# Kernel optimization log

Measured on AMD Instinct MI355X. Metric: run time of the kernel, lower is better.

The kernel has to match this reference:

```python
import jax, jax.numpy as jnp
import numpy as np

NUM_SAMPLE = 10


def setup_inputs() -> dict:
    key = jax.random.key(0)
    k1, k2, k3, k4, k5 = jax.random.split(key, 5)
    N, F, B, S = 100000, 256, 20000, NUM_SAMPLE
    features_ue = jax.random.normal(k1, (N, F), dtype=jnp.float32)
    features_ap = jax.random.normal(k2, (N, F), dtype=jnp.float32)
    neigh_idx = jax.random.randint(k3, (B, S), 0, N, dtype=jnp.int32)
    nodes = jax.random.randint(k4, (B,), 0, N, dtype=jnp.int32)
    # xavier-uniform weight [embed_dim, feature_dim] = [256, 2*F]
    embed_dim, feature_dim = 256, 2 * F
    limit = float(np.sqrt(6.0 / (embed_dim + feature_dim)))
    weight = jax.random.uniform(k5, (embed_dim, feature_dim), dtype=jnp.float32,
                                minval=-limit, maxval=limit)
    return {"features_ue": features_ue, "features_ap": features_ap,
            "neigh_idx": neigh_idx, "nodes": nodes, "weight": weight}


def reference(features_ue, features_ap, neigh_idx, nodes, weight):
    # sample_model='ue2ue': other_feature = self_feature = features_ue
    S = neigh_idx.shape[1]
    # gather sampled neighbor features: [B, S, F] -> sum over S
    gathered = jnp.take(features_ue, neigh_idx, axis=0)
    # original: mask.div(num_neigh + 1), i.e. divide by count PLUS one
    neigh_feats = gathered.sum(axis=1) / jnp.float32(S + 1)  # [B, F]
    self_feats = jnp.take(features_ue, nodes, axis=0)        # [B, F]
    combined = jnp.concatenate([self_feats, neigh_feats], axis=1)  # [B, 2F]
    # weight.mm(combined.t()) then relu -> [embed_dim, B]
    out = jax.nn.relu(jnp.einsum('ef,bf->eb', weight, combined))
    return out
```

## Files before the change

kernel.cpp:

```cpp
#include <hip/hip_runtime.h>

typedef __attribute__((ext_vector_type(8))) short short8;
typedef __attribute__((ext_vector_type(4))) float f32x4;

#define B_TOTAL 20000
#define B_PAD   20096
#define NF      256
#define K2      512
#define NS      10

__device__ __forceinline__ unsigned short f2bf(float x) {
    unsigned u = __builtin_bit_cast(unsigned, x);
    u += 0x7FFFu + ((u >> 16) & 1u);
    return (unsigned short)(u >> 16);
}

__global__ __launch_bounds__(256) void gather_combine(
    const float* __restrict__ ue, const int* __restrict__ nidx,
    const int* __restrict__ nodes, const float* __restrict__ w,
    unsigned short* __restrict__ comb, unsigned short* __restrict__ wbf)
{
    const int t = threadIdx.x, blk = blockIdx.x;
    if (blk < 128) {
        const int base = blk * 1024 + t * 4;
        const float4 v = *(const float4*)(w + base);
        ushort4 o;
        o.x = f2bf(v.x); o.y = f2bf(v.y); o.z = f2bf(v.z); o.w = f2bf(v.w);
        *(ushort4*)(wbf + base) = o;
    }
    const int lane = t & 63;
    const int b = blk * 4 + (t >> 6);
    if (b >= B_PAD) return;
    unsigned short* crow = comb + (size_t)b * K2;
    if (b < B_TOTAL) {
        const int node = nodes[b];
        const float4 sf = ((const float4*)(ue + (size_t)node * NF))[lane];
        int myidx = 0;
        if (lane < NS) myidx = nidx[b * NS + lane];
        float ax = 0.f, ay = 0.f, az = 0.f, aw = 0.f;
        #pragma unroll
        for (int s = 0; s < NS; ++s) {
            const int is = __shfl(myidx, s);
            const float4 v = ((const float4*)(ue + (size_t)is * NF))[lane];
            ax += v.x; ay += v.y; az += v.z; aw += v.w;
        }
        const float inv = 1.0f / 11.0f;
        ushort4 s4, n4;
        s4.x = f2bf(sf.x); s4.y = f2bf(sf.y); s4.z = f2bf(sf.z); s4.w = f2bf(sf.w);
        n4.x = f2bf(ax * inv); n4.y = f2bf(ay * inv); n4.z = f2bf(az * inv); n4.w = f2bf(aw * inv);
        *(ushort4*)(crow + lane * 4) = s4;
        *(ushort4*)(crow + NF + lane * 4) = n4;
    } else {
        ushort4 z; z.x = z.y = z.z = z.w = 0;
        *(ushort4*)(crow + lane * 4) = z;
        *(ushort4*)(crow + NF + lane * 4) = z;
    }
}

__global__ __launch_bounds__(256) void gemm_relu(
    const unsigned short* __restrict__ wbf,
    const unsigned short* __restrict__ comb,
    float* __restrict__ out)
{
    __shared__ unsigned short Alds[4096];
    __shared__ unsigned short Blds[4096];
    const int t    = threadIdx.x;
    const int lane = t & 63;
    const int wv   = t >> 6;
    const int wm   = wv >> 1, wn = wv & 1;
    const int n0   = blockIdx.x * 128;
    const int m0   = blockIdx.y * 128;
    const int srow = t & 127;
    const int skg  = t >> 7;
    const int fr   = lane & 15;
    const int kq   = lane >> 4;

    f32x4 acc[4][4] = {};

    const short8* A8 = (const short8*)Alds;
    const short8* B8 = (const short8*)Blds;

    for (int ks = 0; ks < 16; ++ks) {
        const unsigned short* ga = wbf  + (size_t)(m0 + srow) * K2 + ks * 32 + skg * 8;
        const unsigned short* gb = comb + (size_t)(n0 + srow) * K2 + ks * 32 + skg * 8;
        unsigned short* la = Alds + t * 8;
        unsigned short* lb = Blds + t * 8;
        __builtin_amdgcn_global_load_lds((const __attribute__((address_space(1))) void*)ga,
            (__attribute__((address_space(3))) void*)la, 16, 0, 0);
        __builtin_amdgcn_global_load_lds((const __attribute__((address_space(1))) void*)(ga + 16),
            (__attribute__((address_space(3))) void*)(la + 2048), 16, 0, 0);
        __builtin_amdgcn_global_load_lds((const __attribute__((address_space(1))) void*)gb,
            (__attribute__((address_space(3))) void*)lb, 16, 0, 0);
        __builtin_amdgcn_global_load_lds((const __attribute__((address_space(1))) void*)(gb + 16),
            (__attribute__((address_space(3))) void*)(lb + 2048), 16, 0, 0);
        asm volatile("s_waitcnt vmcnt(0)" ::: "memory");
        __syncthreads();

        short8 af[4], bg[4];
        #pragma unroll
        for (int i = 0; i < 4; ++i)
            af[i] = A8[kq * 128 + wm * 64 + i * 16 + fr];
        #pragma unroll
        for (int j = 0; j < 4; ++j)
            bg[j] = B8[kq * 128 + wn * 64 + j * 16 + fr];
        #pragma unroll
        for (int i = 0; i < 4; ++i)
            #pragma unroll
            for (int j = 0; j < 4; ++j)
                acc[i][j] = __builtin_amdgcn_mfma_f32_16x16x32_bf16(af[i], bg[j], acc[i][j], 0, 0, 0);
        __syncthreads();
    }

    #pragma unroll
    for (int i = 0; i < 4; ++i) {
        const int e = m0 + wm * 64 + i * 16 + kq * 4;
        #pragma unroll
        for (int j = 0; j < 4; ++j) {
            const int b = n0 + wn * 64 + j * 16 + fr;
            if (b < B_TOTAL) {
                #pragma unroll
                for (int r = 0; r < 4; ++r)
                    out[(size_t)(e + r) * B_TOTAL + b] = fmaxf(acc[i][j][r], 0.0f);
            }
        }
    }
}

extern "C" void kernel_launch(void* const* d_in, const int* in_sizes, int n_in,
                              void* d_out, int out_size, void* d_ws, size_t ws_size,
                              hipStream_t stream) {
    const float* ue    = (const float*)d_in[0];
    const int*   nidx  = (const int*)d_in[2];
    const int*   nodes = (const int*)d_in[3];
    const float* w     = (const float*)d_in[4];
    float*       out   = (float*)d_out;

    unsigned short* comb = (unsigned short*)d_ws;
    unsigned short* wbf  = comb + (size_t)B_PAD * K2;

    hipLaunchKernelGGL(gather_combine, dim3(B_PAD / 4), dim3(256), 0, stream,
                       ue, nidx, nodes, w, comb, wbf);
    hipLaunchKernelGGL(gemm_relu, dim3(B_PAD / 128, 2), dim3(256), 0, stream,
                       wbf, comb, out);
}
```

Measured before the change: 60.64 us.

## Restructure GEMM to stage full-K comb tile in LDS and read weights from global

Each block now covers a 64-column slice of comb and computes all 256 output rows. The block loads its full K=512 comb tile into LDS once, in two halves, and starts MFMAs on the first half while the second half is still arriving. Weight fragments are read directly from global memory (L2-resident) instead of being staged in LDS. This removes the per-K-step sync and LDS staging loop and means comb is read once rather than twice. In exchange it uses 64KB of LDS per block, which limits occupancy, and relies on global-memory latency for the weight loads.

```diff
diff --git a/kernel.cpp b/kernel.cpp
--- a/kernel.cpp
+++ b/kernel.cpp
@@ -47,7 +47,8 @@
         const float inv = 1.0f / 11.0f;
         ushort4 s4, n4;
         s4.x = f2bf(sf.x); s4.y = f2bf(sf.y); s4.z = f2bf(sf.z); s4.w = f2bf(sf.w);
-        n4.x = f2bf(ax * inv); n4.y = f2bf(ay * inv); n4.z = f2bf(az * inv); n4.w = f2bf(aw * inv);
+        n4.x = f2bf(ax * inv); n4.y = f2bf(ay * inv);
+        n4.z = f2bf(az * inv); n4.w = f2bf(aw * inv);
         *(ushort4*)(crow + lane * 4) = s4;
         *(ushort4*)(crow + NF + lane * 4) = n4;
     } else {
@@ -62,61 +63,74 @@
     const unsigned short* __restrict__ comb,
     float* __restrict__ out)
 {
-    __shared__ unsigned short Alds[4096];
-    __shared__ unsigned short Blds[4096];
+    __shared__ unsigned short Blds[64 * K2];
     const int t    = threadIdx.x;
     const int lane = t & 63;
     const int wv   = t >> 6;
-    const int wm   = wv >> 1, wn = wv & 1;
-    const int n0   = blockIdx.x * 128;
-    const int m0   = blockIdx.y * 128;
-    const int srow = t & 127;
-    const int skg  = t >> 7;
+    const int n0   = blockIdx.x * 64;
     const int fr   = lane & 15;
     const int kq   = lane >> 4;
 
+    #pragma unroll
+    for (int L = 0; L < 16; ++L) {
+        const int kg = L * 4 + wv;
+        const unsigned short* src = comb + (size_t)(n0 + lane) * K2 + kg * 8;
+        __builtin_amdgcn_global_load_lds(
+            (const __attribute__((address_space(1))) void*)src,
+            (__attribute__((address_space(3))) void*)(Blds + ((size_t)kg * 64 + lane) * 8),
+            16, 0, 0);
+    }
+
+    asm volatile("s_waitcnt vmcnt(8)" ::: "memory");
+    __builtin_amdgcn_s_barrier();
+    __builtin_amdgcn_sched_barrier(0);
+
+    const unsigned short* wp = wbf + (size_t)(wv * 64 + fr) * K2 + kq * 8;
+    const short8* B8 = (const short8*)Blds;
     f32x4 acc[4][4] = {};
 
-    const short8* A8 = (const short8*)Alds;
-    const short8* B8 = (const short8*)Blds;
-
-    for (int ks = 0; ks < 16; ++ks) {
-        const unsigned short* ga = wbf  + (size_t)(m0 + srow) * K2 + ks * 32 + skg * 8;
-        const unsigned short* gb = comb + (size_t)(n0 + srow) * K2 + ks * 32 + skg * 8;
-        unsigned short* la = Alds + t * 8;
-        unsigned short* lb = Blds + t * 8;
-        __builtin_amdgcn_global_load_lds((const __attribute__((address_space(1))) void*)ga,
-            (__attribute__((address_space(3))) void*)la, 16, 0, 0);
-        __builtin_amdgcn_global_load_lds((const __attribute__((address_space(1))) void*)(ga + 16),
-            (__attribute__((address_space(3))) void*)(la + 2048), 16, 0, 0);
-        __builtin_amdgcn_global_load_lds((const __attribute__((address_space(1))) void*)gb,
-            (__attribute__((address_space(3))) void*)lb, 16, 0, 0);
-        __builtin_amdgcn_global_load_lds((const __attribute__((address_space(1))) void*)(gb + 16),
-            (__attribute__((address_space(3))) void*)(lb + 2048), 16, 0, 0);
-        asm volatile("s_waitcnt vmcnt(0)" ::: "memory");
-        __syncthreads();
-
+    #pragma unroll 4
+    for (int ks = 0; ks < 8; ++ks) {
         short8 af[4], bg[4];
         #pragma unroll
         for (int i = 0; i < 4; ++i)
-            af[i] = A8[kq * 128 + wm * 64 + i * 16 + fr];
+            af[i] = *(const short8*)(wp + (size_t)i * 16 * K2 + ks * 32);
         #pragma unroll
         for (int j = 0; j < 4; ++j)
-            bg[j] = B8[kq * 128 + wn * 64 + j * 16 + fr];
+            bg[j] = B8[(ks * 4 + kq) * 64 + j * 16 + fr];
         #pragma unroll
         for (int i = 0; i < 4; ++i)
             #pragma unroll
             for (int j = 0; j < 4; ++j)
                 acc[i][j] = __builtin_amdgcn_mfma_f32_16x16x32_bf16(af[i], bg[j], acc[i][j], 0, 0, 0);
-        __syncthreads();
+    }
+
+    asm volatile("s_waitcnt vmcnt(0)" ::: "memory");
+    __builtin_amdgcn_s_barrier();
+    __builtin_amdgcn_sched_barrier(0);
+
+    #pragma unroll 4
+    for (int ks = 8; ks < 16; ++ks) {
+        short8 af[4], bg[4];
+        #pragma unroll
+        for (int i = 0; i < 4; ++i)
+            af[i] = *(const short8*)(wp + (size_t)i * 16 * K2 + ks * 32);
+        #pragma unroll
+        for (int j = 0; j < 4; ++j)
+            bg[j] = B8[(ks * 4 + kq) * 64 + j * 16 + fr];
+        #pragma unroll
+        for (int i = 0; i < 4; ++i)
+            #pragma unroll
+            for (int j = 0; j < 4; ++j)
+                acc[i][j] = __builtin_amdgcn_mfma_f32_16x16x32_bf16(af[i], bg[j], acc[i][j], 0, 0, 0);
     }
 
     #pragma unroll
     for (int i = 0; i < 4; ++i) {
-        const int e = m0 + wm * 64 + i * 16 + kq * 4;
+        const int e = wv * 64 + i * 16 + kq * 4;
         #pragma unroll
         for (int j = 0; j < 4; ++j) {
-            const int b = n0 + wn * 64 + j * 16 + fr;
+            const int b = n0 + j * 16 + fr;
             if (b < B_TOTAL) {
                 #pragma unroll
                 for (int r = 0; r < 4; ++r)
@@ -140,6 +154,6 @@
 
     hipLaunchKernelGGL(gather_combine, dim3(B_PAD / 4), dim3(256), 0, stream,
                        ue, nidx, nodes, w, comb, wbf);
-    hipLaunchKernelGGL(gemm_relu, dim3(B_PAD / 128, 2), dim3(256), 0, stream,
+    hipLaunchKernelGGL(gemm_relu, dim3(B_PAD / 64), dim3(256), 0, stream,
                        wbf, comb, out);
 }
```

Measured after the change: 64.74 us. +6.8%, slower.
